# Performance work log

Hardware: AMD Instinct MI355X
Metric: run time of the kernel (lower is better)

The kernel has to match this reference:

```python
import jax, jax.numpy as jnp
import numpy as np

EPS = 1e-07

def squash(s, axis=-1):
    sq = jnp.sum(s * s, axis=axis)                      # squared norm
    norm = jnp.sqrt(sq + EPS)
    factor = sq / (1.0 + sq)
    return (factor / norm)[..., None] * s

def setup_inputs() -> dict:
    key = jax.random.key(0)
    k1, = jax.random.split(key, 1)
    B, O, H, W, I, D = 8, 32, 32, 32, 16, 16
    pred = jax.random.normal(k1, (B, O, H, W, I, D), dtype=jnp.float32)
    b = jnp.zeros((1, O, H, W, I), dtype=jnp.float32)
    return {"tensor_of_prediction_vector": pred, "b": b, "num_iterations": 3}

def reference(tensor_of_prediction_vector, b, num_iterations):
    pred = tensor_of_prediction_vector                   # [B,O,H,W,I,D]
    c = jax.nn.softmax(b, axis=-1)                       # [1,O,H,W,I]
    out = squash(jnp.sum(pred * c[..., None], axis=-2))  # [B,O,H,W,D]
    b_batch = b
    for _ in range(num_iterations):
        # agreement: <pred, out> over caps dim D -> [B,O,H,W,I]
        b_batch = b_batch + jnp.sum(pred * out[..., None, :], axis=-1)
        c = jax.nn.softmax(b_batch, axis=-1)
        out = squash(jnp.sum(pred * c[..., None], axis=-2))
    return out
```

## Files before the change

### kernel.cpp

```cpp
#include <hip/hip_runtime.h>

#define DPP_XOR1        0xB1
#define DPP_XOR2        0x4E
#define DPP_HALF_MIRROR 0x141
#define DPP_ROW_MIRROR  0x140

template <int CTRL>
__device__ __forceinline__ float dppf(float x) {
    int i = __builtin_bit_cast(int, x);
    int o = __builtin_amdgcn_update_dpp(0, i, CTRL, 0xF, 0xF, true);
    return __builtin_bit_cast(float, o);
}

__device__ __forceinline__ float allmax16(float v) {
    v = fmaxf(v, dppf<DPP_XOR1>(v));
    v = fmaxf(v, dppf<DPP_XOR2>(v));
    v = fmaxf(v, dppf<DPP_HALF_MIRROR>(v));
    v = fmaxf(v, dppf<DPP_ROW_MIRROR>(v));
    return v;
}

__device__ __forceinline__ float allsum16(float v) {
    v += dppf<DPP_XOR1>(v);
    v += dppf<DPP_XOR2>(v);
    v += dppf<DPP_HALF_MIRROR>(v);
    v += dppf<DPP_ROW_MIRROR>(v);
    return v;
}

__global__ __launch_bounds__(256, 6)
void caps_route_kernel(const float* __restrict__ pred,
                       const float* __restrict__ bias,
                       const int* __restrict__ nitp,
                       float* __restrict__ out,
                       int nsites, int bsites) {
    const int tid  = threadIdx.x;
    const int r    = tid & 15;
    const int site = (blockIdx.x << 4) + (tid >> 4);
    if (site >= nsites) return;
    const int nit = nitp[0];

    const float4* p4 = reinterpret_cast<const float4*>(pred) + ((size_t)site << 6) + (r << 2);
    float4 q0 = p4[0], q1 = p4[1], q2 = p4[2], q3 = p4[3];
    float P[16] = {q0.x, q0.y, q0.z, q0.w,
                   q1.x, q1.y, q1.z, q1.w,
                   q2.x, q2.y, q2.z, q2.w,
                   q3.x, q3.y, q3.z, q3.w};

    float bi = bias[(size_t)(site % bsites) * 16 + r];

    const bool h8 = (r & 8) != 0;
    const bool h4 = (r & 4) != 0;
    const bool h2 = (r & 2) != 0;
    const bool h1 = (r & 1) != 0;

    float o_val = 0.0f;

    auto route_out = [&]() {
        float m = allmax16(bi);
        float e = __expf(bi - m);
        float S = allsum16(e);

        float t[16];
        #pragma unroll
        for (int d = 0; d < 16; ++d) t[d] = e * P[d];

        #pragma unroll
        for (int d = 0; d < 16; ++d) t[d] += dppf<DPP_ROW_MIRROR>(t[d]);
        #pragma unroll
        for (int k = 0; k < 8; ++k) t[k] = h8 ? t[k + 8] : t[k];
        #pragma unroll
        for (int d = 0; d < 8; ++d) t[d] += dppf<DPP_HALF_MIRROR>(t[d]);
        #pragma unroll
        for (int k = 0; k < 4; ++k) t[k] = h4 ? t[k + 4] : t[k];
        #pragma unroll
        for (int d = 0; d < 4; ++d) t[d] += dppf<DPP_XOR2>(t[d]);
        #pragma unroll
        for (int k = 0; k < 2; ++k) t[k] = h2 ? t[k + 2] : t[k];
        #pragma unroll
        for (int d = 0; d < 2; ++d) t[d] += dppf<DPP_XOR1>(t[d]);

        float s_val = (h1 ? t[1] : t[0]) * __builtin_amdgcn_rcpf(S);

        float nsq = allsum16(s_val * s_val);
        float factor = nsq * __builtin_amdgcn_rsqf(nsq + 1e-7f) *
                       __builtin_amdgcn_rcpf(1.0f + nsq);
        o_val = s_val * factor;
    };

    route_out();

    for (int it = 0; it < nit; ++it) {
        float A[16];
        {
            float g = dppf<DPP_XOR1>(o_val);
            A[0] = h1 ? g : o_val;
            A[1] = h1 ? o_val : g;
        }
        {
            float g0 = dppf<DPP_XOR2>(A[0]);
            float g1 = dppf<DPP_XOR2>(A[1]);
            A[2] = h2 ? A[0] : g0;
            A[3] = h2 ? A[1] : g1;
            A[0] = h2 ? g0 : A[0];
            A[1] = h2 ? g1 : A[1];
        }
        {
            float g0 = dppf<DPP_HALF_MIRROR>(A[0]);
            float g1 = dppf<DPP_HALF_MIRROR>(A[1]);
            float g2 = dppf<DPP_HALF_MIRROR>(A[2]);
            float g3 = dppf<DPP_HALF_MIRROR>(A[3]);
            A[4] = h4 ? A[0] : g0;
            A[5] = h4 ? A[1] : g1;
            A[6] = h4 ? A[2] : g2;
            A[7] = h4 ? A[3] : g3;
            A[0] = h4 ? g0 : A[0];
            A[1] = h4 ? g1 : A[1];
            A[2] = h4 ? g2 : A[2];
            A[3] = h4 ? g3 : A[3];
        }
        {
            float g0 = dppf<DPP_ROW_MIRROR>(A[0]);
            float g1 = dppf<DPP_ROW_MIRROR>(A[1]);
            float g2 = dppf<DPP_ROW_MIRROR>(A[2]);
            float g3 = dppf<DPP_ROW_MIRROR>(A[3]);
            float g4 = dppf<DPP_ROW_MIRROR>(A[4]);
            float g5 = dppf<DPP_ROW_MIRROR>(A[5]);
            float g6 = dppf<DPP_ROW_MIRROR>(A[6]);
            float g7 = dppf<DPP_ROW_MIRROR>(A[7]);
            A[8]  = h8 ? A[0] : g0;
            A[9]  = h8 ? A[1] : g1;
            A[10] = h8 ? A[2] : g2;
            A[11] = h8 ? A[3] : g3;
            A[12] = h8 ? A[4] : g4;
            A[13] = h8 ? A[5] : g5;
            A[14] = h8 ? A[6] : g6;
            A[15] = h8 ? A[7] : g7;
            A[0] = h8 ? g0 : A[0];
            A[1] = h8 ? g1 : A[1];
            A[2] = h8 ? g2 : A[2];
            A[3] = h8 ? g3 : A[3];
            A[4] = h8 ? g4 : A[4];
            A[5] = h8 ? g5 : A[5];
            A[6] = h8 ? g6 : A[6];
            A[7] = h8 ? g7 : A[7];
        }

        float agr = 0.0f;
        #pragma unroll
        for (int d = 0; d < 16; ++d) agr = fmaf(P[d], A[d], agr);
        bi += agr;

        route_out();
    }

    out[((size_t)site << 4) + r] = o_val;
}

extern "C" void kernel_launch(void* const* d_in, const int* in_sizes, int n_in,
                              void* d_out, int out_size, void* d_ws, size_t ws_size,
                              hipStream_t stream) {
    const float* pred = (const float*)d_in[0];
    const float* bias = (const float*)d_in[1];
    const int*   nit  = (const int*)d_in[2];
    float* outp = (float*)d_out;

    const int nsites = in_sizes[0] >> 8;
    const int bsites = in_sizes[1] >> 4;

    const int sites_per_block = 16;
    dim3 block(256);
    dim3 grid((nsites + sites_per_block - 1) / sites_per_block);
    caps_route_kernel<<<grid, block, 0, stream>>>(pred, bias, nit, outp, nsites, bsites);
}
```

Before: 403.9 us.

## Replace DPP broadcast with ds_bpermute, drop softmax max, use 2D grid

Replaces the 16-wide DPP/select broadcast of the output vector with 16 ds_bpermute reads, and removes the softmax max-subtraction by exponentiating the logits directly. It also folds the 1/S normalization into the squash scale, launches a 2D grid (bias sites by batch) to avoid the per-thread modulo, and lowers the launch-bounds occupancy hint from 6 to 4. Dropping the max-subtraction risks overflow if the routing logits grow large, and bpermute goes through the LDS crossbar rather than pure VALU.

```diff
diff --git a/kernel.cpp b/kernel.cpp
--- a/kernel.cpp
+++ b/kernel.cpp
@@ -12,14 +12,6 @@
     return __builtin_bit_cast(float, o);
 }
 
-__device__ __forceinline__ float allmax16(float v) {
-    v = fmaxf(v, dppf<DPP_XOR1>(v));
-    v = fmaxf(v, dppf<DPP_XOR2>(v));
-    v = fmaxf(v, dppf<DPP_HALF_MIRROR>(v));
-    v = fmaxf(v, dppf<DPP_ROW_MIRROR>(v));
-    return v;
-}
-
 __device__ __forceinline__ float allsum16(float v) {
     v += dppf<DPP_XOR1>(v);
     v += dppf<DPP_XOR2>(v);
@@ -28,26 +20,27 @@
     return v;
 }
 
-__global__ __launch_bounds__(256, 6)
+__global__ __launch_bounds__(256, 4)
 void caps_route_kernel(const float* __restrict__ pred,
                        const float* __restrict__ bias,
                        const int* __restrict__ nitp,
                        float* __restrict__ out,
-                       int nsites, int bsites) {
-    const int tid  = threadIdx.x;
-    const int r    = tid & 15;
-    const int site = (blockIdx.x << 4) + (tid >> 4);
-    if (site >= nsites) return;
+                       int bsites) {
+    const int tid   = threadIdx.x;
+    const int r     = tid & 15;
+    const int bsite = (blockIdx.x << 4) + (tid >> 4);
+    if (bsite >= bsites) return;
+    const size_t site = (size_t)blockIdx.y * bsites + bsite;
     const int nit = nitp[0];
 
-    const float4* p4 = reinterpret_cast<const float4*>(pred) + ((size_t)site << 6) + (r << 2);
+    const float4* p4 = reinterpret_cast<const float4*>(pred) + (site << 6) + (r << 2);
     float4 q0 = p4[0], q1 = p4[1], q2 = p4[2], q3 = p4[3];
     float P[16] = {q0.x, q0.y, q0.z, q0.w,
                    q1.x, q1.y, q1.z, q1.w,
                    q2.x, q2.y, q2.z, q2.w,
                    q3.x, q3.y, q3.z, q3.w};
 
-    float bi = bias[(size_t)(site % bsites) * 16 + r];
+    float bi = bias[((size_t)bsite << 4) + r];
 
     const bool h8 = (r & 8) != 0;
     const bool h4 = (r & 4) != 0;
@@ -57,8 +50,7 @@
     float o_val = 0.0f;
 
     auto route_out = [&]() {
-        float m = allmax16(bi);
-        float e = __expf(bi - m);
+        float e = __expf(bi);
         float S = allsum16(e);
 
         float t[16];
@@ -79,82 +71,33 @@
         for (int k = 0; k < 2; ++k) t[k] = h2 ? t[k + 2] : t[k];
         #pragma unroll
         for (int d = 0; d < 2; ++d) t[d] += dppf<DPP_XOR1>(t[d]);
+        float u = h1 ? t[1] : t[0];
 
-        float s_val = (h1 ? t[1] : t[0]) * __builtin_amdgcn_rcpf(S);
-
-        float nsq = allsum16(s_val * s_val);
-        float factor = nsq * __builtin_amdgcn_rsqf(nsq + 1e-7f) *
-                       __builtin_amdgcn_rcpf(1.0f + nsq);
-        o_val = s_val * factor;
+        float rS  = __builtin_amdgcn_rcpf(S);
+        float nsq = allsum16(u * u) * rS * rS;
+        float k_s = rS * nsq * __builtin_amdgcn_rsqf(nsq + 1e-7f) *
+                    __builtin_amdgcn_rcpf(1.0f + nsq);
+        o_val = u * k_s;
     };
 
     route_out();
 
+    const int gbase = (tid & 48) << 2;
+
     for (int it = 0; it < nit; ++it) {
-        float A[16];
-        {
-            float g = dppf<DPP_XOR1>(o_val);
-            A[0] = h1 ? g : o_val;
-            A[1] = h1 ? o_val : g;
-        }
-        {
-            float g0 = dppf<DPP_XOR2>(A[0]);
-            float g1 = dppf<DPP_XOR2>(A[1]);
-            A[2] = h2 ? A[0] : g0;
-            A[3] = h2 ? A[1] : g1;
-            A[0] = h2 ? g0 : A[0];
-            A[1] = h2 ? g1 : A[1];
-        }
-        {
-            float g0 = dppf<DPP_HALF_MIRROR>(A[0]);
-            float g1 = dppf<DPP_HALF_MIRROR>(A[1]);
-            float g2 = dppf<DPP_HALF_MIRROR>(A[2]);
-            float g3 = dppf<DPP_HALF_MIRROR>(A[3]);
-            A[4] = h4 ? A[0] : g0;
-            A[5] = h4 ? A[1] : g1;
-            A[6] = h4 ? A[2] : g2;
-            A[7] = h4 ? A[3] : g3;
-            A[0] = h4 ? g0 : A[0];
-            A[1] = h4 ? g1 : A[1];
-            A[2] = h4 ? g2 : A[2];
-            A[3] = h4 ? g3 : A[3];
-        }
-        {
-            float g0 = dppf<DPP_ROW_MIRROR>(A[0]);
-            float g1 = dppf<DPP_ROW_MIRROR>(A[1]);
-            float g2 = dppf<DPP_ROW_MIRROR>(A[2]);
-            float g3 = dppf<DPP_ROW_MIRROR>(A[3]);
-            float g4 = dppf<DPP_ROW_MIRROR>(A[4]);
-            float g5 = dppf<DPP_ROW_MIRROR>(A[5]);
-            float g6 = dppf<DPP_ROW_MIRROR>(A[6]);
-            float g7 = dppf<DPP_ROW_MIRROR>(A[7]);
-            A[8]  = h8 ? A[0] : g0;
-            A[9]  = h8 ? A[1] : g1;
-            A[10] = h8 ? A[2] : g2;
-            A[11] = h8 ? A[3] : g3;
-            A[12] = h8 ? A[4] : g4;
-            A[13] = h8 ? A[5] : g5;
-            A[14] = h8 ? A[6] : g6;
-            A[15] = h8 ? A[7] : g7;
-            A[0] = h8 ? g0 : A[0];
-            A[1] = h8 ? g1 : A[1];
-            A[2] = h8 ? g2 : A[2];
-            A[3] = h8 ? g3 : A[3];
-            A[4] = h8 ? g4 : A[4];
-            A[5] = h8 ? g5 : A[5];
-            A[6] = h8 ? g6 : A[6];
-            A[7] = h8 ? g7 : A[7];
-        }
-
+        const int ov = __builtin_bit_cast(int, o_val);
         float agr = 0.0f;
         #pragma unroll
-        for (int d = 0; d < 16; ++d) agr = fmaf(P[d], A[d], agr);
+        for (int j = 0; j < 16; ++j) {
+            float Aj = __builtin_bit_cast(float,
+                        __builtin_amdgcn_ds_bpermute(gbase + (j << 2), ov));
+            agr = fmaf(P[j], Aj, agr);
+        }
         bi += agr;
-
         route_out();
     }
 
-    out[((size_t)site << 4) + r] = o_val;
+    out[(site << 4) + r] = o_val;
 }
 
 extern "C" void kernel_launch(void* const* d_in, const int* in_sizes, int n_in,
@@ -165,11 +108,10 @@
     const int*   nit  = (const int*)d_in[2];
     float* outp = (float*)d_out;
 
-    const int nsites = in_sizes[0] >> 8;
     const int bsites = in_sizes[1] >> 4;
+    const int batch  = (int)(((size_t)in_sizes[0] >> 8) / (size_t)bsites);
 
-    const int sites_per_block = 16;
     dim3 block(256);
-    dim3 grid((nsites + sites_per_block - 1) / sites_per_block);
-    caps_route_kernel<<<grid, block, 0, stream>>>(pred, bias, nit, outp, nsites, bsites);
+    dim3 grid((bsites + 15) / 16, batch);
+    caps_route_kernel<<<grid, block, 0, stream>>>(pred, bias, nit, outp, bsites);
 }
```

After: 403.3 us. Within noise of the previous version (-0.1%).
